# Kernel optimization log

Hardware: AMD Instinct MI355X
Metric: run time of the kernel (lower is better)

## Reference

```python
import jax, jax.numpy as jnp
import numpy as np

B, T, D, R = 4, 2048, 512, 1024
N_INNER, N_B = 9, 2          # inner pool bins, boundary pool bins (roipool_size='2_9')
RATIO = 1.0 / 5.0            # boundary extension ratio passed to BRoI1DPool
NB = N_B + N_INNER + N_B     # 13 total bins: [start bins | inner bins | end bins]


def _bin_centers(a, b, n):
    # a, b: (B, R) -> (B, R, n) centers of n equal bins covering [a, b]
    i = (jnp.arange(n, dtype=a.dtype) + 0.5) / n
    return a[..., None] + i * (b - a)[..., None]


def broi1d_pool(feats, rois):
    # Boundary ROI 1D pooling: feats (B, T, D), rois (B, R, 2) -> (B, R, D, NB).
    # Each bin samples its center position via linear interpolation along T.
    s, e = rois[..., 0], rois[..., 1]
    ext = RATIO * (e - s)
    pos = jnp.concatenate([
        _bin_centers(s - ext, s + ext, N_B),
        _bin_centers(s, e, N_INNER),
        _bin_centers(e - ext, e + ext, N_B)], axis=-1)          # (B, R, NB)
    pos = jnp.clip(pos, 0.0, T - 1)
    lo = jnp.floor(pos).astype(jnp.int32)
    hi = jnp.minimum(lo + 1, T - 1)
    w = (pos - lo.astype(pos.dtype))[..., None]

    def gather(idx):
        g = jnp.take_along_axis(feats, idx.reshape(idx.shape[0], -1)[..., None], axis=1)
        return g.reshape(idx.shape + (feats.shape[-1],))          # (B, R, NB, D)

    vals = (1.0 - w) * gather(lo) + w * gather(hi)
    return vals.transpose(0, 1, 3, 2)                              # (B, R, D, NB)


def setup_inputs():
    key = jax.random.key(0)
    ks = jax.random.split(key, 10)
    features = jax.random.normal(ks[0], (B, T, D), jnp.float32)

    def make_rois(k):
        k1, k2 = jax.random.split(k)
        s = jax.random.uniform(k1, (B, R), jnp.float32, 0.0, T - 300.0)
        L = 16.0 + jax.random.uniform(k2, (B, R), jnp.float32) * 256.0
        return jnp.stack([s, s + L], axis=-1)

    rois = make_rois(ks[1])
    start_rois = make_rois(ks[2])
    end_rois = make_rois(ks[3])
    rois_mask = jnp.ones((B, R), jnp.float32)
    rois_pos_emb = jax.random.normal(ks[4], (B, R, D), jnp.float32)

    d_left = (N_B + N_INNER // 2 + 1) * D
    W_left = jax.random.normal(ks[5], (D, d_left), jnp.float32) / np.sqrt(d_left).astype(np.float32)
    b_left = jnp.zeros((D,), jnp.float32)
    W_inner = jax.random.normal(ks[6], (D, N_INNER * D), jnp.float32) / np.sqrt(N_INNER * D).astype(np.float32)
    b_inner = jnp.zeros((D,), jnp.float32)
    W_roi = jax.random.normal(ks[7], (D, 2 * D), jnp.float32) / np.sqrt(2 * D).astype(np.float32)
    b_roi = jnp.zeros((D,), jnp.float32)
    return {"features": features, "start_rois": start_rois, "end_rois": end_rois,
            "rois": rois, "rois_mask": rois_mask, "rois_pos_emb": rois_pos_emb,
            "W_left": W_left, "b_left": b_left, "W_inner": W_inner, "b_inner": b_inner,
            "W_roi": W_roi, "b_roi": b_roi}


def reference(features, start_rois, end_rois, rois, rois_mask, rois_pos_emb,
              W_left, b_left, W_inner, b_inner, W_roi, b_roi):
    pooled = broi1d_pool(features, rois)          # (B, R, D, NB)
    mb, r = pooled.shape[:2]

    def fc(x, W, b):
        # Linear + Dropout(eval=identity) + SELU
        return jax.nn.selu(x @ W.T + b)

    left = fc(pooled[:, :, :, 0:N_INNER // 2 + N_B + 1].reshape(mb, r, -1), W_left, b_left)
    inner = fc(pooled[:, :, :, N_B:N_INNER + N_B].reshape(mb, r, -1), W_inner, b_inner)
    # NOTE: the original code reuses left_fc for the right branch (right_fc is dead).
    right = fc(pooled[:, :, :, N_INNER // 2 + N_B:N_INNER + 2 * N_B].reshape(mb, r, -1), W_left, b_left)
    return fc(jnp.concatenate([right - left, inner], axis=2), W_roi, b_roi)  # (B, R, D)
```

## Files before the change

kernel.cpp:

```cpp
#include <hip/hip_runtime.h>
#include <hip/hip_bf16.h>
#include <cstdint>
#include <cmath>

#define BB 4
#define TT 2048
#define DD 512
#define RR 1024
#define MM (BB*RR)
#define NBINS 13
#define LDXP (NBINS*DD)

typedef __bf16 bf16;
typedef bf16 bf16x8 __attribute__((ext_vector_type(8)));
typedef bf16 bf16x2 __attribute__((ext_vector_type(2)));
typedef float f32x4 __attribute__((ext_vector_type(4)));

__device__ __forceinline__ float selu_f(float x) {
    const float sc = 1.0507009873554805f;
    const float aa = 1.6732632423543772f;
    return x > 0.0f ? sc * x : sc * aa * (expf(x) - 1.0f);
}

__device__ __forceinline__ void gload_lds16(const bf16* g, bf16* l) {
    __builtin_amdgcn_global_load_lds(
        (const __attribute__((address_space(1))) void*)g,
        (__attribute__((address_space(3))) void*)l, 16, 0, 0);
}

__device__ __forceinline__ void waitb() {
    asm volatile("s_waitcnt vmcnt(0)" ::: "memory");
    __builtin_amdgcn_s_barrier();
}

template<int ROWS>
__device__ __forceinline__ void stage_tile64(const bf16* __restrict__ src, int lda,
                                             bf16* tile, int tid) {
#pragma unroll
    for (int it = 0; it < ROWS / 32; ++it) {
        int idx = it * 256 + tid;
        int row = idx >> 3;
        int col = ((idx & 7) ^ (row & 7)) * 8;
        bf16* wavebase = tile + (idx & ~63) * 8;
        gload_lds16(src + (size_t)row * lda + col, wavebase);
    }
}

__device__ __forceinline__ bf16x8 frd64(const bf16* tile, int row, int s) {
    int p = s ^ (row & 7);
    return *(const bf16x8*)(tile + row * 64 + p * 8);
}

template<int NB_, int KT>
__device__ __forceinline__ void w_interleave_body(const float* __restrict__ Wsrc,
                                                  bf16* __restrict__ Wdst, int i) {
    int n = i / KT;
    int t = i - n * KT;
    int bin = t >> 9;
    int d = t & 511;
    Wdst[i] = (bf16)Wsrc[(size_t)n * KT + (size_t)d * NB_ + bin];
}

__device__ __forceinline__ void pool_body(const float* __restrict__ feats,
                                          const float* __restrict__ rois,
                                          bf16* __restrict__ Xp, int m, int tid) {
    int b = m >> 10;
    float s = rois[2 * m];
    float e = rois[2 * m + 1];
    float ext = 0.2f * (e - s);
    int d0 = tid * 2;
    bf16* orow = Xp + (size_t)m * LDXP + d0;
    const float* fb = feats + (size_t)b * TT * DD + d0;
#pragma unroll
    for (int j = 0; j < NBINS; ++j) {
        float pos;
        if (j < 2)       pos = (s - ext) + ((float)j + 0.5f) * ext;
        else if (j < 11) pos = s + (((float)(j - 2) + 0.5f) * (1.0f / 9.0f)) * (e - s);
        else             pos = (e - ext) + ((float)(j - 11) + 0.5f) * ext;
        pos = fminf(fmaxf(pos, 0.0f), (float)(TT - 1));
        float fl = floorf(pos);
        int lo = (int)fl;
        int hi = lo + 1; if (hi > TT - 1) hi = TT - 1;
        float w = pos - fl;
        float2 vlo = *(const float2*)(fb + (size_t)lo * DD);
        float2 vhi = *(const float2*)(fb + (size_t)hi * DD);
        bf16x2 o;
        o.x = (bf16)((1.0f - w) * vlo.x + w * vhi.x);
        o.y = (bf16)((1.0f - w) * vlo.y + w * vhi.y);
        *(bf16x2*)(orow + j * DD) = o;
    }
}

__global__ __launch_bounds__(256) void prep_all(
    const float* __restrict__ feats, const float* __restrict__ rois,
    const float* __restrict__ W_left, const float* __restrict__ W_inner,
    const float* __restrict__ W_roi,
    bf16* __restrict__ Xp, bf16* __restrict__ Wl, bf16* __restrict__ Wi,
    bf16* __restrict__ Wr)
{
    int bid = blockIdx.x, tid = threadIdx.x;
    if (bid < 4096) {
        pool_body(feats, rois, Xp, bid, tid);
    } else if (bid < 4096 + 7168) {
        int i = (bid - 4096) * 256 + tid;
        w_interleave_body<7, 3584>(W_left, Wl, i);
    } else if (bid < 4096 + 7168 + 9216) {
        int i = (bid - 11264) * 256 + tid;
        w_interleave_body<9, 4608>(W_inner, Wi, i);
    } else {
        int i = (bid - 20480) * 256 + tid;
        Wr[i] = (bf16)W_roi[i];
    }
}


template<int K, bool OUT_BF16>
__device__ __forceinline__ void gemm_single_body(
    const bf16* __restrict__ A, int lda,
    const bf16* __restrict__ Bw, const float* __restrict__ bias,
    void* __restrict__ Out, int ldo, int ocol0,
    bf16* sm, int m0, int n0)
{
    int tid = threadIdx.x, lane = tid & 63, w = tid >> 6;
    int wr = w >> 1, wc = w & 1;
    const bf16* Ab = A + (size_t)m0 * lda;
    const bf16* Bb = Bw + (size_t)n0 * K;
    int frow = lane & 15, sl = lane >> 4;
    f32x4 acc[2][4] = {};
    bf16 *A0 = sm,         *B0 = sm + 4096;
    bf16 *A1 = sm + 12288, *B1 = sm + 12288 + 4096;

    auto stage = [&](bf16* as, bf16* bs, int t) {
        stage_tile64<64>(Ab + t * 64, lda, as, tid);
        stage_tile64<128>(Bb + t * 64, K, bs, tid);
    };
    auto compute = [&](const bf16* as, const bf16* bs) {
#pragma unroll
        for (int ks = 0; ks < 2; ++ks) {
            bf16x8 af[2], bfr[4];
#pragma unroll
            for (int mf = 0; mf < 2; ++mf) af[mf] = frd64(as, wr * 32 + mf * 16 + frow, ks * 4 + sl);
#pragma unroll
            for (int nf = 0; nf < 4; ++nf) bfr[nf] = frd64(bs, wc * 64 + nf * 16 + frow, ks * 4 + sl);
            __builtin_amdgcn_s_setprio(1);
#pragma unroll
            for (int mf = 0; mf < 2; ++mf)
#pragma unroll
                for (int nf = 0; nf < 4; ++nf)
                    acc[mf][nf] = __builtin_amdgcn_mfma_f32_16x16x32_bf16(af[mf], bfr[nf], acc[mf][nf], 0, 0, 0);
            __builtin_amdgcn_s_setprio(0);
        }
    };

    constexpr int NT = K / 64;
    stage(A0, B0, 0);
    waitb();
    for (int t = 0; t < NT; t += 2) {
        stage(A1, B1, t + 1);
        compute(A0, B0);
        waitb();
        if (t + 2 < NT) stage(A0, B0, t + 2);
        compute(A1, B1);
        waitb();
    }
    int crow = (lane >> 4) * 4;
    int ccol = lane & 15;
#pragma unroll
    for (int mf = 0; mf < 2; ++mf) {
#pragma unroll
        for (int nf = 0; nf < 4; ++nf) {
            int col = n0 + wc * 64 + nf * 16 + ccol;
            float bv = bias[col];
#pragma unroll
            for (int r2 = 0; r2 < 4; ++r2) {
                int row = m0 + wr * 32 + mf * 16 + crow + r2;
                float v = selu_f(acc[mf][nf][r2] + bv);
                if constexpr (OUT_BF16)
                    ((bf16*)Out)[(size_t)row * ldo + ocol0 + col] = (bf16)v;
                else
                    ((float*)Out)[(size_t)row * ldo + ocol0 + col] = v;
            }
        }
    }
}

template<int K>
__device__ __forceinline__ void gemm_dual_body(
    const bf16* __restrict__ Xp, const bf16* __restrict__ Wl,
    const float* __restrict__ bias, bf16* __restrict__ Y,
    bf16* sm, int m0, int n0)
{
    int tid = threadIdx.x, lane = tid & 63, w = tid >> 6;
    int wr = w >> 1, wc = w & 1;
    const bf16* AL = Xp + (size_t)m0 * LDXP;
    const bf16* AR = AL + 3072;
    const bf16* Bb = Wl + (size_t)n0 * K;
    int frow = lane & 15, sl = lane >> 4;
    f32x4 accL[2][4] = {}, accR[2][4] = {};
    bf16 *L0 = sm,         *R0 = sm + 4096,         *B0 = sm + 8192;
    bf16 *L1 = sm + 16384, *R1 = sm + 16384 + 4096, *B1 = sm + 16384 + 8192;

    auto stage = [&](bf16* ls, bf16* rs, bf16* bs, int t) {
        stage_tile64<64>(AL + t * 64, LDXP, ls, tid);
        stage_tile64<64>(AR + t * 64, LDXP, rs, tid);
        stage_tile64<128>(Bb + t * 64, K, bs, tid);
    };
    auto compute = [&](const bf16* ls, const bf16* rs, const bf16* bs) {
#pragma unroll
        for (int ks = 0; ks < 2; ++ks) {
            bf16x8 afL[2], afR[2], bfr[4];
#pragma unroll
            for (int mf = 0; mf < 2; ++mf) {
                afL[mf] = frd64(ls, wr * 32 + mf * 16 + frow, ks * 4 + sl);
                afR[mf] = frd64(rs, wr * 32 + mf * 16 + frow, ks * 4 + sl);
            }
#pragma unroll
            for (int nf = 0; nf < 4; ++nf) bfr[nf] = frd64(bs, wc * 64 + nf * 16 + frow, ks * 4 + sl);
            __builtin_amdgcn_s_setprio(1);
#pragma unroll
            for (int mf = 0; mf < 2; ++mf)
#pragma unroll
                for (int nf = 0; nf < 4; ++nf) {
                    accL[mf][nf] = __builtin_amdgcn_mfma_f32_16x16x32_bf16(afL[mf], bfr[nf], accL[mf][nf], 0, 0, 0);
                    accR[mf][nf] = __builtin_amdgcn_mfma_f32_16x16x32_bf16(afR[mf], bfr[nf], accR[mf][nf], 0, 0, 0);
                }
            __builtin_amdgcn_s_setprio(0);
        }
    };

    constexpr int NT = K / 64;
    stage(L0, R0, B0, 0);
    waitb();
    for (int t = 0; t < NT; t += 2) {
        stage(L1, R1, B1, t + 1);
        compute(L0, R0, B0);
        waitb();
        if (t + 2 < NT) stage(L0, R0, B0, t + 2);
        compute(L1, R1, B1);
        waitb();
    }
    int crow = (lane >> 4) * 4;
    int ccol = lane & 15;
#pragma unroll
    for (int mf = 0; mf < 2; ++mf) {
#pragma unroll
        for (int nf = 0; nf < 4; ++nf) {
            int col = n0 + wc * 64 + nf * 16 + ccol;
            float bv = bias[col];
#pragma unroll
            for (int r2 = 0; r2 < 4; ++r2) {
                int row = m0 + wr * 32 + mf * 16 + crow + r2;
                float vL = selu_f(accL[mf][nf][r2] + bv);
                float vR = selu_f(accR[mf][nf][r2] + bv);
                Y[(size_t)row * 1024 + col] = (bf16)(vR - vL);
            }
        }
    }
}

__global__ __launch_bounds__(256) void wide_gemm(
    const bf16* __restrict__ Xp, const bf16* __restrict__ Wl,
    const float* __restrict__ bl, const bf16* __restrict__ Wi,
    const float* __restrict__ bi, bf16* __restrict__ Y)
{
    __shared__ bf16 sm[32768];
    int bid = blockIdx.x;
    if (bid < 256) {
        gemm_dual_body<3584>(Xp, Wl, bl, Y, sm, (bid & 63) * 64, (bid >> 6) * 128);
    } else {
        int b2 = bid - 256;
        gemm_single_body<4608, true>(Xp + 1024, LDXP, Wi, bi, (void*)Y, 1024, 512,
                                     sm, (b2 & 63) * 64, (b2 >> 6) * 128);
    }
}

__global__ __launch_bounds__(256) void final_gemm(
    const bf16* __restrict__ Y, const bf16* __restrict__ Wr,
    const float* __restrict__ br, float* __restrict__ out)
{
    __shared__ bf16 sm[24576];
    int bid = blockIdx.x;
    gemm_single_body<1024, false>(Y, 1024, Wr, br, (void*)out, 512, 0,
                                  sm, (bid & 63) * 64, (bid >> 6) * 128);
}

extern "C" void kernel_launch(void* const* d_in, const int* in_sizes, int n_in,
                              void* d_out, int out_size, void* d_ws, size_t ws_size,
                              hipStream_t stream) {
    const float* feats   = (const float*)d_in[0];
    const float* rois    = (const float*)d_in[3];
    const float* W_left  = (const float*)d_in[6];
    const float* b_left  = (const float*)d_in[7];
    const float* W_inner = (const float*)d_in[8];
    const float* b_inner = (const float*)d_in[9];
    const float* W_roi   = (const float*)d_in[10];
    const float* b_roi   = (const float*)d_in[11];
    float* out = (float*)d_out;

    bf16* wsb = (bf16*)d_ws;
    constexpr size_t XP_ELEMS = (size_t)MM * LDXP;
    constexpr size_t WL_ELEMS = (size_t)512 * 3584;
    constexpr size_t WI_ELEMS = (size_t)512 * 4608;
    constexpr size_t WR_ELEMS = (size_t)512 * 1024;
    bf16* Xp = wsb;
    bf16* Wl = Xp + XP_ELEMS;
    bf16* Wi = Wl + WL_ELEMS;
    bf16* Wr = Wi + WI_ELEMS;
    bf16* Y  = Wr + WR_ELEMS;

    prep_all<<<22528, 256, 0, stream>>>(feats, rois, W_left, W_inner, W_roi,
                                        Xp, Wl, Wi, Wr);
    wide_gemm<<<512, 256, 0, stream>>>(Xp, Wl, b_left, Wi, b_inner, Y);
    final_gemm<<<256, 256, 0, stream>>>(Y, Wr, b_roi, out);
}
```

Measured before the change: 111.7 us.

## Pipeline GEMM loads with partial vmcnt waits and row-staged weight interleave

The GEMM main loops now keep two tiles in flight and wait only until the older tile's loads have landed, using partial vmcnt counts instead of full drains, so loads overlap compute. The weight-interleave step in the prep kernel now processes one weight row per block: it stages the row in shared memory and writes it out coalesced, replacing strided per-element global gathers. The W_roi conversion is vectorised with float4 loads, which shrinks the prep grid. The risk is that the vmcnt counts must exactly match the loads issued per stage, and the new 18KB shared array applies to every prep block, including the pooling blocks, which may lower occupancy.

```diff
diff --git a/kernel.cpp b/kernel.cpp
--- a/kernel.cpp
+++ b/kernel.cpp
@@ -28,9 +28,11 @@
         (__attribute__((address_space(3))) void*)l, 16, 0, 0);
 }
 
-__device__ __forceinline__ void waitb() {
-    asm volatile("s_waitcnt vmcnt(0)" ::: "memory");
-    __builtin_amdgcn_s_barrier();
+template<int N>
+__device__ __forceinline__ void wait_vm() {
+    if constexpr (N == 0)      asm volatile("s_waitcnt vmcnt(0)" ::: "memory");
+    else if constexpr (N == 6) asm volatile("s_waitcnt vmcnt(6)" ::: "memory");
+    else if constexpr (N == 8) asm volatile("s_waitcnt vmcnt(8)" ::: "memory");
 }
 
 template<int ROWS>
@@ -52,13 +54,17 @@
 }
 
 template<int NB_, int KT>
-__device__ __forceinline__ void w_interleave_body(const float* __restrict__ Wsrc,
-                                                  bf16* __restrict__ Wdst, int i) {
-    int n = i / KT;
-    int t = i - n * KT;
-    int bin = t >> 9;
-    int d = t & 511;
-    Wdst[i] = (bf16)Wsrc[(size_t)n * KT + (size_t)d * NB_ + bin];
+__device__ __forceinline__ void w_row_body(const float* __restrict__ Wsrc,
+                                           bf16* __restrict__ Wdst,
+                                           float* ld, int n, int tid) {
+    const float* src = Wsrc + (size_t)n * KT;
+    for (int i = tid; i < KT; i += 256) ld[i] = src[i];
+    __syncthreads();
+    bf16* dst = Wdst + (size_t)n * KT;
+    for (int i = tid; i < KT; i += 256) {
+        int bin = i >> 9, d = i & 511;
+        dst[i] = (bf16)ld[d * NB_ + bin];
+    }
 }
 
 __device__ __forceinline__ void pool_body(const float* __restrict__ feats,
@@ -98,18 +104,19 @@
     bf16* __restrict__ Xp, bf16* __restrict__ Wl, bf16* __restrict__ Wi,
     bf16* __restrict__ Wr)
 {
+    __shared__ float ld[4608];
     int bid = blockIdx.x, tid = threadIdx.x;
     if (bid < 4096) {
         pool_body(feats, rois, Xp, bid, tid);
-    } else if (bid < 4096 + 7168) {
-        int i = (bid - 4096) * 256 + tid;
-        w_interleave_body<7, 3584>(W_left, Wl, i);
-    } else if (bid < 4096 + 7168 + 9216) {
-        int i = (bid - 11264) * 256 + tid;
-        w_interleave_body<9, 4608>(W_inner, Wi, i);
+    } else if (bid < 4608) {
+        w_row_body<7, 3584>(W_left, Wl, ld, bid - 4096, tid);
+    } else if (bid < 5120) {
+        w_row_body<9, 4608>(W_inner, Wi, ld, bid - 4608, tid);
     } else {
-        int i = (bid - 20480) * 256 + tid;
-        Wr[i] = (bf16)W_roi[i];
+        int i0 = (bid - 5120) * 1024 + tid * 4;
+        float4 v = *(const float4*)(W_roi + i0);
+        bf16* d = Wr + i0;
+        d[0] = (bf16)v.x; d[1] = (bf16)v.y; d[2] = (bf16)v.z; d[3] = (bf16)v.w;
     }
 }
 
@@ -154,15 +161,19 @@
 
     constexpr int NT = K / 64;
     stage(A0, B0, 0);
-    waitb();
-    for (int t = 0; t < NT; t += 2) {
-        stage(A1, B1, t + 1);
-        compute(A0, B0);
-        waitb();
-        if (t + 2 < NT) stage(A0, B0, t + 2);
-        compute(A1, B1);
-        waitb();
-    }
+    stage(A1, B1, 1);
+    for (int t = 0; t + 2 < NT; ++t) {
+        wait_vm<6>(); __builtin_amdgcn_s_barrier();
+        const bf16 *as = (t & 1) ? A1 : A0, *bs = (t & 1) ? B1 : B0;
+        compute(as, bs);
+        __builtin_amdgcn_s_barrier();
+        stage((t & 1) ? A1 : A0, (t & 1) ? B1 : B0, t + 2);
+    }
+    wait_vm<6>(); __builtin_amdgcn_s_barrier();
+    { const bf16 *as = (NT & 1) ? A1 : A0, *bs = (NT & 1) ? B1 : B0; compute(as, bs); }
+    wait_vm<0>(); __builtin_amdgcn_s_barrier();
+    { const bf16 *as = (NT & 1) ? A0 : A1, *bs = (NT & 1) ? B0 : B1; compute(as, bs); }
+
     int crow = (lane >> 4) * 4;
     int ccol = lane & 15;
 #pragma unroll
@@ -230,15 +241,21 @@
 
     constexpr int NT = K / 64;
     stage(L0, R0, B0, 0);
-    waitb();
-    for (int t = 0; t < NT; t += 2) {
-        stage(L1, R1, B1, t + 1);
-        compute(L0, R0, B0);
-        waitb();
-        if (t + 2 < NT) stage(L0, R0, B0, t + 2);
-        compute(L1, R1, B1);
-        waitb();
-    }
+    stage(L1, R1, B1, 1);
+    for (int t = 0; t + 2 < NT; ++t) {
+        wait_vm<8>(); __builtin_amdgcn_s_barrier();
+        const bf16 *ls = (t & 1) ? L1 : L0, *rs = (t & 1) ? R1 : R0, *bs = (t & 1) ? B1 : B0;
+        compute(ls, rs, bs);
+        __builtin_amdgcn_s_barrier();
+        stage((t & 1) ? L1 : L0, (t & 1) ? R1 : R0, (t & 1) ? B1 : B0, t + 2);
+    }
+    wait_vm<8>(); __builtin_amdgcn_s_barrier();
+    { const bf16 *ls = (NT & 1) ? L1 : L0, *rs = (NT & 1) ? R1 : R0, *bs = (NT & 1) ? B1 : B0;
+      compute(ls, rs, bs); }
+    wait_vm<0>(); __builtin_amdgcn_s_barrier();
+    { const bf16 *ls = (NT & 1) ? L0 : L1, *rs = (NT & 1) ? R0 : R1, *bs = (NT & 1) ? B0 : B1;
+      compute(ls, rs, bs); }
+
     int crow = (lane >> 4) * 4;
     int ccol = lane & 15;
 #pragma unroll
@@ -308,8 +325,8 @@
     bf16* Wr = Wi + WI_ELEMS;
     bf16* Y  = Wr + WR_ELEMS;
 
-    prep_all<<<22528, 256, 0, stream>>>(feats, rois, W_left, W_inner, W_roi,
-                                        Xp, Wl, Wi, Wr);
+    prep_all<<<5632, 256, 0, stream>>>(feats, rois, W_left, W_inner, W_roi,
+                                       Xp, Wl, Wi, Wr);
     wide_gemm<<<512, 256, 0, stream>>>(Xp, Wl, b_left, Wi, b_inner, Y);
     final_gemm<<<256, 256, 0, stream>>>(Y, Wr, b_roi, out);
 }
```

New measurement: 111.7 us. No clear change (-0.0%).

## Stage weight rows in LDS for coalesced transpose and remap GEMM blocks per XCD

Applied to the files above, without the earlier changes.

The weight bin-interleave now loads each full weight row into shared memory with coalesced reads, then writes the permuted bf16 row, where before each thread did a strided scattered global read. W_roi conversion is vectorized with float4 loads. The wide and final GEMM block indices are remapped so blocks on the same XCD share an N-column tile and a contiguous M range, for better L2 reuse of weights. prep_all now reserves 18KB of shared memory for every block, including pool blocks, which may reduce occupancy for the pooling work.

```diff
diff --git a/kernel.cpp b/kernel.cpp
--- a/kernel.cpp
+++ b/kernel.cpp
@@ -52,13 +52,17 @@
 }
 
 template<int NB_, int KT>
-__device__ __forceinline__ void w_interleave_body(const float* __restrict__ Wsrc,
-                                                  bf16* __restrict__ Wdst, int i) {
-    int n = i / KT;
-    int t = i - n * KT;
-    int bin = t >> 9;
-    int d = t & 511;
-    Wdst[i] = (bf16)Wsrc[(size_t)n * KT + (size_t)d * NB_ + bin];
+__device__ __forceinline__ void w_row_body(const float* __restrict__ Wsrc,
+                                           bf16* __restrict__ Wdst,
+                                           float* ld, int n, int tid) {
+    const float* src = Wsrc + (size_t)n * KT;
+    for (int i = tid; i < KT; i += 256) ld[i] = src[i];
+    __syncthreads();
+    bf16* dst = Wdst + (size_t)n * KT;
+    for (int i = tid; i < KT; i += 256) {
+        int bin = i >> 9, d = i & 511;
+        dst[i] = (bf16)ld[d * NB_ + bin];
+    }
 }
 
 __device__ __forceinline__ void pool_body(const float* __restrict__ feats,
@@ -98,18 +102,19 @@
     bf16* __restrict__ Xp, bf16* __restrict__ Wl, bf16* __restrict__ Wi,
     bf16* __restrict__ Wr)
 {
+    __shared__ float ld[4608];
     int bid = blockIdx.x, tid = threadIdx.x;
     if (bid < 4096) {
         pool_body(feats, rois, Xp, bid, tid);
-    } else if (bid < 4096 + 7168) {
-        int i = (bid - 4096) * 256 + tid;
-        w_interleave_body<7, 3584>(W_left, Wl, i);
-    } else if (bid < 4096 + 7168 + 9216) {
-        int i = (bid - 11264) * 256 + tid;
-        w_interleave_body<9, 4608>(W_inner, Wi, i);
+    } else if (bid < 4608) {
+        w_row_body<7, 3584>(W_left, Wl, ld, bid - 4096, tid);
+    } else if (bid < 5120) {
+        w_row_body<9, 4608>(W_inner, Wi, ld, bid - 4608, tid);
     } else {
-        int i = (bid - 20480) * 256 + tid;
-        Wr[i] = (bf16)W_roi[i];
+        int i0 = (bid - 5120) * 1024 + tid * 4;
+        float4 v = *(const float4*)(W_roi + i0);
+        bf16* d = Wr + i0;
+        d[0] = (bf16)v.x; d[1] = (bf16)v.y; d[2] = (bf16)v.z; d[3] = (bf16)v.w;
     }
 }
 
@@ -264,13 +269,16 @@
     const float* __restrict__ bi, bf16* __restrict__ Y)
 {
     __shared__ bf16 sm[32768];
-    int bid = blockIdx.x;
-    if (bid < 256) {
-        gemm_dual_body<3584>(Xp, Wl, bl, Y, sm, (bid & 63) * 64, (bid >> 6) * 128);
+    int b = blockIdx.x;
+    int xcd = b & 7, slot = b >> 3;
+    int n0 = (xcd & 3) * 128;
+    if (slot < 32) {
+        int m0 = ((xcd >> 2) * 32 + slot) * 64;
+        gemm_dual_body<3584>(Xp, Wl, bl, Y, sm, m0, n0);
     } else {
-        int b2 = bid - 256;
+        int m0 = ((xcd >> 2) * 32 + (slot - 32)) * 64;
         gemm_single_body<4608, true>(Xp + 1024, LDXP, Wi, bi, (void*)Y, 1024, 512,
-                                     sm, (b2 & 63) * 64, (b2 >> 6) * 128);
+                                     sm, m0, n0);
     }
 }
 
@@ -279,9 +287,12 @@
     const float* __restrict__ br, float* __restrict__ out)
 {
     __shared__ bf16 sm[24576];
-    int bid = blockIdx.x;
+    int b = blockIdx.x;
+    int xcd = b & 7, slot = b >> 3;
+    int n0 = (xcd & 3) * 128;
+    int m0 = ((xcd >> 2) * 32 + slot) * 64;
     gemm_single_body<1024, false>(Y, 1024, Wr, br, (void*)out, 512, 0,
-                                  sm, (bid & 63) * 64, (bid >> 6) * 128);
+                                  sm, m0, n0);
 }
 
 extern "C" void kernel_launch(void* const* d_in, const int* in_sizes, int n_in,
@@ -308,8 +319,8 @@
     bf16* Wr = Wi + WI_ELEMS;
     bf16* Y  = Wr + WR_ELEMS;
 
-    prep_all<<<22528, 256, 0, stream>>>(feats, rois, W_left, W_inner, W_roi,
-                                        Xp, Wl, Wi, Wr);
+    prep_all<<<5632, 256, 0, stream>>>(feats, rois, W_left, W_inner, W_roi,
+                                       Xp, Wl, Wi, Wr);
     wide_gemm<<<512, 256, 0, stream>>>(Xp, Wl, b_left, Wi, b_inner, Y);
     final_gemm<<<256, 256, 0, stream>>>(Y, Wr, b_roi, out);
 }
```

Result: slower. 120.2 us (+7.6%).
